# Kernel tuning notes

Measured on AMD Instinct MI355X. Metric: run time of the kernel, lower is better.

The kernel has to match this reference:

```python
import jax, jax.numpy as jnp
import numpy as np

N, E, D, H, L, QD = 100000, 640000, 128, 256, 3, 768


def setup_inputs() -> dict:
    key = jax.random.key(0)
    ks = jax.random.split(key, 16)
    def W(k, shape, fan):
        return jax.random.normal(k, shape, jnp.float32) / np.float32(np.sqrt(fan))
    return {
        "node_embedding": jax.random.normal(ks[0], (N, D), jnp.float32),
        "relation_embedding": jax.random.normal(ks[1], (E, D), jnp.float32),
        "question_embedding": jax.random.normal(ks[2], (1, QD), jnp.float32),
        "edge_index": jax.random.randint(ks[3], (2, E), 0, N),
        "edge_type": jax.random.randint(ks[4], (E,), 0, 2000),
        "qW": W(ks[5], (QD, D), QD),
        "qb": jnp.zeros((D,), jnp.float32),
        "eW1": W(ks[6], (L, 4 * D, H), 4 * D),
        "eb1": jnp.zeros((L, H), jnp.float32),
        "eW2": W(ks[7], (L, H, D), H),
        "eb2": jnp.zeros((L, D), jnp.float32),
        "nW1": W(ks[8], (L, 2 * D, H), 2 * D),
        "nb1": jnp.zeros((L, H), jnp.float32),
        "nW2": W(ks[9], (L, H, D), H),
        "nb2": jnp.zeros((L, D), jnp.float32),
        "esW": W(ks[10], (D, 1), D),
        "esb": jnp.zeros((1,), jnp.float32),
        "nsW": W(ks[11], (D, 1), D),
        "nsb": jnp.zeros((1,), jnp.float32),
    }


def reference(node_embedding, relation_embedding, question_embedding, edge_index,
              edge_type, qW, qb, eW1, eb1, eW2, eb2, nW1, nb1, nW2, nb2,
              esW, esb, nsW, nsb):
    # edge_type is unused in the original forward as well.
    q = question_embedding @ qW + qb  # [1, D]
    src, dst = edge_index[0], edge_index[1]
    node_h = node_embedding  # [N, D]
    edge_h = relation_embedding  # [E, D]
    num_layers = eW1.shape[0]
    for l in range(num_layers):
        edge_src = node_h[src]  # gather [E, D]
        edge_dst = node_h[dst]  # gather [E, D]
        q_exp = jnp.broadcast_to(q, (edge_src.shape[0], q.shape[1]))
        edge_feat = jnp.concatenate([edge_src, edge_dst, edge_h, q_exp], axis=-1)  # [E, 4D]
        h = jax.nn.relu(edge_feat @ eW1[l] + eb1[l])
        edge_h = h @ eW2[l] + eb2[l]  # [E, D]
        # scatter-add to both endpoints (index_add_ on src then dst)
        agg = jnp.zeros_like(node_h).at[src].add(edge_h).at[dst].add(edge_h)
        nh = jax.nn.relu(jnp.concatenate([node_h, agg], axis=-1) @ nW1[l] + nb1[l])
        node_h = nh @ nW2[l] + nb2[l]
    edge_scores = jax.nn.sigmoid((edge_h @ esW + esb).squeeze(-1))  # [E]
    node_scores = jax.nn.sigmoid((node_h @ nsW + nsb).squeeze(-1))  # [N]
    return node_scores, edge_scores
```

## Files before the change

### kernel.cpp

```cpp
#include <hip/hip_runtime.h>
#include <math.h>

#define NN 100000
#define NE 640000
#define DD 128
#define HH 256
#define NL 3
#define QDIM 768
#define TM 64

#define A1P 392
#define A2P 264
#define OP  136

typedef _Float16 h16x8 __attribute__((ext_vector_type(8)));
typedef float f32x4 __attribute__((ext_vector_type(4)));

#define MFMA16(A, B, C) __builtin_amdgcn_mfma_f32_16x16x32_f16(A, B, C, 0, 0, 0)

__device__ __forceinline__ unsigned short f2h_bits(float f) {
    _Float16 h = (_Float16)f;
    return __builtin_bit_cast(unsigned short, h);
}
__device__ __forceinline__ unsigned pk2(float a, float b) {
    return (unsigned)f2h_bits(a) | ((unsigned)f2h_bits(b) << 16);
}
__device__ __forceinline__ float h2f(unsigned short u) {
    return (float)__builtin_bit_cast(_Float16, u);
}

__global__ void q_kernel(const float* __restrict__ qe, const float* __restrict__ qW,
                         const float* __restrict__ qb, float* __restrict__ q) {
    int d = threadIdx.x;
    float acc = qb[d];
    for (int k = 0; k < QDIM; ++k) acc = fmaf(qe[k], qW[k * DD + d], acc);
    q[d] = acc;
}

__global__ void qc_kernel(const float* __restrict__ q, const float* __restrict__ eW1,
                          const float* __restrict__ eb1, float* __restrict__ qc) {
    int l = blockIdx.x;
    int h = threadIdx.x;
    const float* W = eW1 + ((size_t)l * 4 * DD + 3 * DD) * HH;
    __shared__ float sq[DD];
    if (h < DD) sq[h] = q[h];
    __syncthreads();
    float acc = eb1[l * HH + h];
    for (int d = 0; d < DD; ++d) acc = fmaf(sq[d], W[d * HH + h], acc);
    qc[l * HH + h] = acc;
}

__global__ void pack_kernel(const float* __restrict__ W, unsigned short* __restrict__ out,
                            int K, int Ncols, int lstride, size_t plane ) {
    int nct = Ncols >> 4;
    int bx = blockIdx.x;
    int l = blockIdx.y;
    int lane = threadIdx.x;
    const float* Wl = W + (size_t)l * lstride;
    int kt = bx / nct, ct = bx - kt * nct;
    int r = kt * 32 + (lane >> 4) * 8;
    int c = ct * 16 + (lane & 15);
    unsigned vh[4], vl[4];
#pragma unroll
    for (int p = 0; p < 4; ++p) {
        float x0 = Wl[(size_t)(r + 2 * p) * Ncols + c];
        float x1 = Wl[(size_t)(r + 2 * p + 1) * Ncols + c];
        _Float16 h0 = (_Float16)x0, h1 = (_Float16)x1;
        _Float16 l0 = (_Float16)(x0 - (float)h0), l1 = (_Float16)(x1 - (float)h1);
        vh[p] = (unsigned)__builtin_bit_cast(unsigned short, h0) |
                ((unsigned)__builtin_bit_cast(unsigned short, h1) << 16);
        vl[p] = (unsigned)__builtin_bit_cast(unsigned short, l0) |
                ((unsigned)__builtin_bit_cast(unsigned short, l1) << 16);
    }
    size_t off = (size_t)l * K * Ncols + ((size_t)bx * 64 + lane) * 8;
    *(uint4*)(out + off) = make_uint4(vh[0], vh[1], vh[2], vh[3]);
    *(uint4*)(out + plane + off) = make_uint4(vl[0], vl[1], vl[2], vl[3]);
}

__global__ void deg_kernel(const int* __restrict__ eidx, int* __restrict__ cnt) {
    int i = blockIdx.x * 256 + threadIdx.x;
    if (i < 2 * NE) atomicAdd(&cnt[eidx[i]], 1);
}

#define SCAN_T 1024
__global__ void scan_kernel(const int* __restrict__ cnt, int* __restrict__ offsets,
                            int* __restrict__ cursor) {
    __shared__ int s[SCAN_T];
    int t = threadIdx.x;
    const int chunk = (NN + SCAN_T - 1) / SCAN_T;
    int lo = t * chunk, hi = lo + chunk; if (hi > NN) hi = NN;
    int sum = 0;
    for (int i = lo; i < hi; ++i) sum += cnt[i];
    s[t] = sum;
    __syncthreads();
    for (int off = 1; off < SCAN_T; off <<= 1) {
        int v = (t >= off) ? s[t - off] : 0;
        __syncthreads();
        s[t] += v;
        __syncthreads();
    }
    int run = (t == 0) ? 0 : s[t - 1];
    for (int i = lo; i < hi; ++i) {
        int c = cnt[i];
        offsets[i] = run;
        cursor[i] = run;
        run += c;
    }
    if (t == SCAN_T - 1) offsets[NN] = run;
}

__global__ void fill_kernel(const int* __restrict__ eidx, int* __restrict__ cursor,
                            int* __restrict__ inc) {
    int i = blockIdx.x * 256 + threadIdx.x;
    if (i < 2 * NE) {
        int e = (i < NE) ? i : i - NE;
        int pos = atomicAdd(&cursor[eidx[i]], 1);
        inc[pos] = e;
    }
}

template <bool IN16>
__global__ __launch_bounds__(256, 3) void edge_kernel(
    const void* node_in, const void* edge_in,
    unsigned short* edge_out,
    const int* __restrict__ eidx,
    const unsigned short* __restrict__ W1hi, const unsigned short* __restrict__ W1lo,
    const float* __restrict__ qc,
    const unsigned short* __restrict__ W2hi, const unsigned short* __restrict__ W2lo,
    const float* __restrict__ b2)
{
    __shared__ unsigned short sA[TM * A1P];
    unsigned short* sA1 = sA;
    unsigned short* sA2 = sA;
    unsigned short* sOut = sA;

    const int tid = threadIdx.x;
    const int e0 = blockIdx.x * TM;

    const int row = tid >> 2, t4 = tid & 3;
    const int srcn = eidx[e0 + row];
    const int dstn = eidx[NE + e0 + row];

    if (IN16) {
        const unsigned short* b0 = (const unsigned short*)node_in + (size_t)srcn * 256;
        const unsigned short* b1 = (const unsigned short*)node_in + (size_t)dstn * 256;
        const unsigned short* bp = (const unsigned short*)edge_in + (size_t)(e0 + row) * 256;
#pragma unroll
        for (int i = 0; i < 12; ++i) {
            int seg = i >> 2, j = i & 3;
            int c = (t4 + 4 * j) * 8;
            const unsigned short* g = (seg == 0) ? b0 : (seg == 1) ? b1 : bp;
            *(uint4*)&sA1[row * A1P + seg * 128 + c] = *(const uint4*)(g + c);
        }
    } else {
        const float* b0 = (const float*)node_in + (size_t)srcn * DD;
        const float* b1 = (const float*)node_in + (size_t)dstn * DD;
        const float* bp = (const float*)edge_in + (size_t)(e0 + row) * DD;
#pragma unroll
        for (int i = 0; i < 12; ++i) {
            int seg = i >> 2, j = i & 3;
            int c = (t4 + 4 * j) * 8;
            const float* g = (seg == 0) ? b0 : (seg == 1) ? b1 : bp;
            float4 v0 = *(const float4*)(g + c);
            float4 v1 = *(const float4*)(g + c + 4);
            uint4 p = make_uint4(pk2(v0.x, v0.y), pk2(v0.z, v0.w),
                                 pk2(v1.x, v1.y), pk2(v1.z, v1.w));
            *(uint4*)&sA1[row * A1P + seg * 128 + c] = p;
        }
    }

    const int lane = tid & 63;
    const int w = tid >> 6;
    const int lrow = lane & 15;
    const int q4 = lane >> 4;

    f32x4 acc[4][4];
#pragma unroll
    for (int ct = 0; ct < 4; ++ct) {
        float iv = qc[w * 64 + ct * 16 + lrow];
        f32x4 c = {iv, iv, iv, iv};
#pragma unroll
        for (int rt = 0; rt < 4; ++rt) acc[rt][ct] = c;
    }
    __syncthreads();

    const h16x8* W1h = (const h16x8*)W1hi;
    const h16x8* W1l = (const h16x8*)W1lo;
    for (int kt = 0; kt < 12; ++kt) {
        h16x8 a[4];
#pragma unroll
        for (int rt = 0; rt < 4; ++rt)
            a[rt] = *(const h16x8*)&sA1[(lrow + 16 * rt) * A1P + kt * 32 + q4 * 8];
#pragma unroll
        for (int ct = 0; ct < 4; ++ct) {
            h16x8 bh = W1h[(kt * 16 + w * 4 + ct) * 64 + lane];
            h16x8 bl = W1l[(kt * 16 + w * 4 + ct) * 64 + lane];
#pragma unroll
            for (int rt = 0; rt < 4; ++rt) {
                acc[rt][ct] = MFMA16(a[rt], bh, acc[rt][ct]);
                acc[rt][ct] = MFMA16(a[rt], bl, acc[rt][ct]);
            }
        }
    }

    __syncthreads();

#pragma unroll
    for (int rt = 0; rt < 4; ++rt)
#pragma unroll
        for (int ct = 0; ct < 4; ++ct)
#pragma unroll
            for (int j = 0; j < 4; ++j) {
                int hr = rt * 16 + q4 * 4 + j;
                int hc = w * 64 + ct * 16 + lrow;
                sA2[hr * A2P + hc] = f2h_bits(fmaxf(acc[rt][ct][j], 0.0f));
            }
    __syncthreads();

    f32x4 acc2[4][2];
#pragma unroll
    for (int ct = 0; ct < 2; ++ct) {
        float iv = b2[w * 32 + ct * 16 + lrow];
        f32x4 c = {iv, iv, iv, iv};
#pragma unroll
        for (int rt = 0; rt < 4; ++rt) acc2[rt][ct] = c;
    }
    const h16x8* W2h = (const h16x8*)W2hi;
    const h16x8* W2l = (const h16x8*)W2lo;
    for (int kt = 0; kt < 8; ++kt) {
        h16x8 a[4];
#pragma unroll
        for (int rt = 0; rt < 4; ++rt)
            a[rt] = *(const h16x8*)&sA2[(lrow + 16 * rt) * A2P + kt * 32 + q4 * 8];
#pragma unroll
        for (int ct = 0; ct < 2; ++ct) {
            h16x8 bh = W2h[(kt * 8 + w * 2 + ct) * 64 + lane];
            h16x8 bl = W2l[(kt * 8 + w * 2 + ct) * 64 + lane];
#pragma unroll
            for (int rt = 0; rt < 4; ++rt) {
                acc2[rt][ct] = MFMA16(a[rt], bh, acc2[rt][ct]);
                acc2[rt][ct] = MFMA16(a[rt], bl, acc2[rt][ct]);
            }
        }
    }

    __syncthreads();
#pragma unroll
    for (int rt = 0; rt < 4; ++rt)
#pragma unroll
        for (int j = 0; j < 4; ++j) {
            int rr = rt * 16 + q4 * 4 + j;
#pragma unroll
            for (int ct = 0; ct < 2; ++ct)
                sOut[rr * OP + w * 32 + ct * 16 + lrow] = f2h_bits(acc2[rt][ct][j]);
        }
    __syncthreads();
    {
        unsigned short* er = edge_out + (size_t)(e0 + row) * 256;
#pragma unroll
        for (int j = 0; j < 4; ++j)
            *(uint4*)(er + t4 * 32 + j * 8) = *(const uint4*)&sOut[row * OP + t4 * 32 + j * 8];
    }
}

template <bool IN16>
__global__ __launch_bounds__(256, 3) void node_kernel(
    const void* node_in, unsigned short* node_out,
    const unsigned short* __restrict__ edge16,
    const int* __restrict__ offsets, const int* __restrict__ inc,
    const unsigned short* __restrict__ W1hi, const unsigned short* __restrict__ W1lo,
    const float* __restrict__ b1,
    const unsigned short* __restrict__ W2hi, const unsigned short* __restrict__ W2lo,
    const float* __restrict__ b2)
{
    __shared__ unsigned short sA[TM * A2P];
    unsigned short* sA1 = sA;
    unsigned short* sA2 = sA;
    unsigned short* sOut = sA;

    const int tid = threadIdx.x;
    const int n0 = blockIdx.x * TM;

    const int row = tid >> 2, t4 = tid & 3;
    const int n = n0 + row;
    const bool vrow = (n < NN);

    if (vrow) {
        if (IN16) {
            const unsigned short* g0 = (const unsigned short*)node_in + (size_t)n * 256;
#pragma unroll
            for (int j = 0; j < 4; ++j) {
                int c = t4 * 32 + j * 8;
                *(uint4*)&sA1[row * A2P + c] = *(const uint4*)(g0 + c);
            }
        } else {
            const float* g0 = (const float*)node_in + (size_t)n * DD;
#pragma unroll
            for (int j = 0; j < 4; ++j) {
                int c = t4 * 32 + j * 8;
                float4 v0 = *(const float4*)(g0 + c);
                float4 v1 = *(const float4*)(g0 + c + 4);
                uint4 p = make_uint4(pk2(v0.x, v0.y), pk2(v0.z, v0.w),
                                     pk2(v1.x, v1.y), pk2(v1.z, v1.w));
                *(uint4*)&sA1[row * A2P + c] = p;
            }
        }
    } else {
        uint4 z = make_uint4(0, 0, 0, 0);
#pragma unroll
        for (int j = 0; j < 4; ++j)
            *(uint4*)&sA1[row * A2P + t4 * 32 + j * 8] = z;
    }

    {
        int k0 = 0, k1 = 0;
        if (vrow) { k0 = offsets[n]; k1 = offsets[n + 1]; }
        float a[32];
#pragma unroll
        for (int j = 0; j < 32; ++j) a[j] = 0.0f;
        for (int k = k0; k < k1; ++k) {
            int e = inc[k];
            const unsigned short* er = edge16 + (size_t)e * 256 + t4 * 32;
#pragma unroll
            for (int j = 0; j < 4; ++j) {
                uint4 v = *(const uint4*)(er + j * 8);
                a[j * 8 + 0] += h2f((unsigned short)(v.x & 0xffff));
                a[j * 8 + 1] += h2f((unsigned short)(v.x >> 16));
                a[j * 8 + 2] += h2f((unsigned short)(v.y & 0xffff));
                a[j * 8 + 3] += h2f((unsigned short)(v.y >> 16));
                a[j * 8 + 4] += h2f((unsigned short)(v.z & 0xffff));
                a[j * 8 + 5] += h2f((unsigned short)(v.z >> 16));
                a[j * 8 + 6] += h2f((unsigned short)(v.w & 0xffff));
                a[j * 8 + 7] += h2f((unsigned short)(v.w >> 16));
            }
        }
#pragma unroll
        for (int j = 0; j < 4; ++j) {
            uint4 p = make_uint4(pk2(a[j * 8 + 0], a[j * 8 + 1]), pk2(a[j * 8 + 2], a[j * 8 + 3]),
                                 pk2(a[j * 8 + 4], a[j * 8 + 5]), pk2(a[j * 8 + 6], a[j * 8 + 7]));
            *(uint4*)&sA1[row * A2P + 128 + t4 * 32 + j * 8] = p;
        }
    }

    const int lane = tid & 63;
    const int w = tid >> 6;
    const int lrow = lane & 15;
    const int q4 = lane >> 4;

    f32x4 acc[4][4];
#pragma unroll
    for (int ct = 0; ct < 4; ++ct) {
        float iv = b1[w * 64 + ct * 16 + lrow];
        f32x4 c = {iv, iv, iv, iv};
#pragma unroll
        for (int rt = 0; rt < 4; ++rt) acc[rt][ct] = c;
    }
    __syncthreads();

    const h16x8* W1h = (const h16x8*)W1hi;
    const h16x8* W1l = (const h16x8*)W1lo;
    for (int kt = 0; kt < 8; ++kt) {
        h16x8 a[4];
#pragma unroll
        for (int rt = 0; rt < 4; ++rt)
            a[rt] = *(const h16x8*)&sA1[(lrow + 16 * rt) * A2P + kt * 32 + q4 * 8];
#pragma unroll
        for (int ct = 0; ct < 4; ++ct) {
            h16x8 bh = W1h[(kt * 16 + w * 4 + ct) * 64 + lane];
            h16x8 bl = W1l[(kt * 16 + w * 4 + ct) * 64 + lane];
#pragma unroll
            for (int rt = 0; rt < 4; ++rt) {
                acc[rt][ct] = MFMA16(a[rt], bh, acc[rt][ct]);
                acc[rt][ct] = MFMA16(a[rt], bl, acc[rt][ct]);
            }
        }
    }

    __syncthreads();

#pragma unroll
    for (int rt = 0; rt < 4; ++rt)
#pragma unroll
        for (int ct = 0; ct < 4; ++ct)
#pragma unroll
            for (int j = 0; j < 4; ++j) {
                int hr = rt * 16 + q4 * 4 + j;
                int hc = w * 64 + ct * 16 + lrow;
                sA2[hr * A2P + hc] = f2h_bits(fmaxf(acc[rt][ct][j], 0.0f));
            }
    __syncthreads();

    f32x4 acc2[4][2];
#pragma unroll
    for (int ct = 0; ct < 2; ++ct) {
        float iv = b2[w * 32 + ct * 16 + lrow];
        f32x4 c = {iv, iv, iv, iv};
#pragma unroll
        for (int rt = 0; rt < 4; ++rt) acc2[rt][ct] = c;
    }
    const h16x8* W2h = (const h16x8*)W2hi;
    const h16x8* W2l = (const h16x8*)W2lo;
    for (int kt = 0; kt < 8; ++kt) {
        h16x8 a[4];
#pragma unroll
        for (int rt = 0; rt < 4; ++rt)
            a[rt] = *(const h16x8*)&sA2[(lrow + 16 * rt) * A2P + kt * 32 + q4 * 8];
#pragma unroll
        for (int ct = 0; ct < 2; ++ct) {
            h16x8 bh = W2h[(kt * 8 + w * 2 + ct) * 64 + lane];
            h16x8 bl = W2l[(kt * 8 + w * 2 + ct) * 64 + lane];
#pragma unroll
            for (int rt = 0; rt < 4; ++rt) {
                acc2[rt][ct] = MFMA16(a[rt], bh, acc2[rt][ct]);
                acc2[rt][ct] = MFMA16(a[rt], bl, acc2[rt][ct]);
            }
        }
    }

    __syncthreads();
#pragma unroll
    for (int rt = 0; rt < 4; ++rt)
#pragma unroll
        for (int j = 0; j < 4; ++j) {
            int rr = rt * 16 + q4 * 4 + j;
#pragma unroll
            for (int ct = 0; ct < 2; ++ct)
                sOut[rr * OP + w * 32 + ct * 16 + lrow] = f2h_bits(acc2[rt][ct][j]);
        }
    __syncthreads();
    if (vrow) {
        unsigned short* nr = node_out + (size_t)n * 256;
#pragma unroll
        for (int j = 0; j < 4; ++j)
            *(uint4*)(nr + t4 * 32 + j * 8) = *(const uint4*)&sOut[row * OP + t4 * 32 + j * 8];
    }
}

__global__ void score_kernel(const unsigned short* __restrict__ hmat,
                             const float* __restrict__ w,
                             const float* __restrict__ b, float* __restrict__ out) {
    int wid = threadIdx.x >> 6;
    int lane = threadIdx.x & 63;
    int row = blockIdx.x * 4 + wid;
    unsigned v = *(const unsigned*)(hmat + (size_t)row * 256 + lane * 2);
    float2 wv = *(const float2*)(w + lane * 2);
    float s = h2f((unsigned short)(v & 0xffff)) * wv.x +
              h2f((unsigned short)(v >> 16)) * wv.y;
#pragma unroll
    for (int off = 32; off; off >>= 1) s += __shfl_down(s, off);
    if (lane == 0) out[row] = 1.0f / (1.0f + expf(-(s + b[0])));
}

extern "C" void kernel_launch(void* const* d_in, const int* in_sizes, int n_in,
                              void* d_out, int out_size, void* d_ws, size_t ws_size,
                              hipStream_t stream) {
    float* node_h = (float*)d_in[0];
    float* edge_h = (float*)d_in[1];
    const float* qe   = (const float*)d_in[2];
    const int*   eidx = (const int*)d_in[3];
    const float* qW  = (const float*)d_in[5];
    const float* qb  = (const float*)d_in[6];
    const float* eW1 = (const float*)d_in[7];
    const float* eb1 = (const float*)d_in[8];
    const float* eW2 = (const float*)d_in[9];
    const float* eb2 = (const float*)d_in[10];
    const float* nW1 = (const float*)d_in[11];
    const float* nb1 = (const float*)d_in[12];
    const float* nW2 = (const float*)d_in[13];
    const float* nb2 = (const float*)d_in[14];
    const float* esW = (const float*)d_in[15];
    const float* esb = (const float*)d_in[16];
    const float* nsW = (const float*)d_in[17];
    const float* nsb = (const float*)d_in[18];

    unsigned short* nh16 = (unsigned short*)node_h;
    unsigned short* eh16 = (unsigned short*)edge_h;

    float* ws  = (float*)d_ws;
    float* q   = ws;
    float* qc  = ws + 256;
    int* cnt     = (int*)(ws + 1024);
    int* cursor  = cnt + NN;
    int* offsets = cursor + NN;
    int* inc     = offsets + NN + 1;

    unsigned short* packs = (unsigned short*)d_out;
    const size_t pe1 = (size_t)NL * 384 * 256;
    const size_t pe2 = (size_t)NL * 256 * 128;
    const size_t pn1 = (size_t)NL * 256 * 256;
    const size_t pn2 = (size_t)NL * 256 * 128;
    unsigned short* eW1p = packs;
    unsigned short* eW2p = eW1p + 2 * pe1;
    unsigned short* nW1p = eW2p + 2 * pe2;
    unsigned short* nW2p = nW1p + 2 * pn1;

    q_kernel<<<1, DD, 0, stream>>>(qe, qW, qb, q);
    qc_kernel<<<NL, HH, 0, stream>>>(q, eW1, eb1, qc);
    pack_kernel<<<dim3(12 * 16, NL), 64, 0, stream>>>(eW1, eW1p, 384, 256, 4 * DD * HH, pe1);
    pack_kernel<<<dim3(8 * 8, NL), 64, 0, stream>>>(eW2, eW2p, 256, 128, HH * DD, pe2);
    pack_kernel<<<dim3(8 * 16, NL), 64, 0, stream>>>(nW1, nW1p, 256, 256, 2 * DD * HH, pn1);
    pack_kernel<<<dim3(8 * 8, NL), 64, 0, stream>>>(nW2, nW2p, 256, 128, HH * DD, pn2);

    hipMemsetAsync(cnt, 0, NN * sizeof(int), stream);
    deg_kernel<<<(2 * NE + 255) / 256, 256, 0, stream>>>(eidx, cnt);
    scan_kernel<<<1, SCAN_T, 0, stream>>>(cnt, offsets, cursor);
    fill_kernel<<<(2 * NE + 255) / 256, 256, 0, stream>>>(eidx, cursor, inc);

    for (int l = 0; l < NL; ++l) {
        if (l == 0) {
            edge_kernel<false><<<NE / TM, 256, 0, stream>>>(
                (const void*)node_h, (const void*)edge_h, eh16, eidx,
                eW1p + (size_t)l * 384 * 256, eW1p + pe1 + (size_t)l * 384 * 256,
                qc + l * HH,
                eW2p + (size_t)l * 256 * 128, eW2p + pe2 + (size_t)l * 256 * 128,
                eb2 + l * DD);
            node_kernel<false><<<(NN + TM - 1) / TM, 256, 0, stream>>>(
                (const void*)node_h, nh16, eh16, offsets, inc,
                nW1p + (size_t)l * 256 * 256, nW1p + pn1 + (size_t)l * 256 * 256,
                nb1 + l * HH,
                nW2p + (size_t)l * 256 * 128, nW2p + pn2 + (size_t)l * 256 * 128,
                nb2 + l * DD);
        } else {
            edge_kernel<true><<<NE / TM, 256, 0, stream>>>(
                (const void*)nh16, (const void*)eh16, eh16, eidx,
                eW1p + (size_t)l * 384 * 256, eW1p + pe1 + (size_t)l * 384 * 256,
                qc + l * HH,
                eW2p + (size_t)l * 256 * 128, eW2p + pe2 + (size_t)l * 256 * 128,
                eb2 + l * DD);
            node_kernel<true><<<(NN + TM - 1) / TM, 256, 0, stream>>>(
                (const void*)nh16, nh16, eh16, offsets, inc,
                nW1p + (size_t)l * 256 * 256, nW1p + pn1 + (size_t)l * 256 * 256,
                nb1 + l * HH,
                nW2p + (size_t)l * 256 * 128, nW2p + pn2 + (size_t)l * 256 * 128,
                nb2 + l * DD);
        }
    }

    score_kernel<<<NN / 4, 256, 0, stream>>>(nh16, nsW, nsb, (float*)d_out);
    score_kernel<<<NE / 4, 256, 0, stream>>>(eh16, esW, esb, (float*)d_out + NN);
}
```

Baseline: 2.302 ms.

## Stream contiguous operand rows directly from global memory into MFMA, shrink LDS

```diff
diff --git a/kernel.cpp b/kernel.cpp
--- a/kernel.cpp
+++ b/kernel.cpp
@@ -9,8 +9,7 @@
 #define QDIM 768
 #define TM 64
 
-#define A1P 392
-#define A2P 264
+#define EAP 264
 #define OP  136
 
 typedef _Float16 h16x8 __attribute__((ext_vector_type(8)));
@@ -27,6 +26,12 @@
 }
 __device__ __forceinline__ float h2f(unsigned short u) {
     return (float)__builtin_bit_cast(_Float16, u);
+}
+__device__ __forceinline__ h16x8 f4x2_to_h8(float4 v0, float4 v1) {
+    union { unsigned u[4]; h16x8 h; } u;
+    u.u[0] = pk2(v0.x, v0.y); u.u[1] = pk2(v0.z, v0.w);
+    u.u[2] = pk2(v1.x, v1.y); u.u[3] = pk2(v1.z, v1.w);
+    return u.h;
 }
 
 __global__ void q_kernel(const float* __restrict__ qe, const float* __restrict__ qW,
@@ -120,7 +125,7 @@
 }
 
 template <bool IN16>
-__global__ __launch_bounds__(256, 3) void edge_kernel(
+__global__ __launch_bounds__(256, 4) void edge_kernel(
     const void* node_in, const void* edge_in,
     unsigned short* edge_out,
     const int* __restrict__ eidx,
@@ -129,7 +134,7 @@
     const unsigned short* __restrict__ W2hi, const unsigned short* __restrict__ W2lo,
     const float* __restrict__ b2)
 {
-    __shared__ unsigned short sA[TM * A1P];
+    __shared__ unsigned short sA[TM * EAP];
     unsigned short* sA1 = sA;
     unsigned short* sA2 = sA;
     unsigned short* sOut = sA;
@@ -144,28 +149,27 @@
     if (IN16) {
         const unsigned short* b0 = (const unsigned short*)node_in + (size_t)srcn * 256;
         const unsigned short* b1 = (const unsigned short*)node_in + (size_t)dstn * 256;
-        const unsigned short* bp = (const unsigned short*)edge_in + (size_t)(e0 + row) * 256;
-#pragma unroll
-        for (int i = 0; i < 12; ++i) {
-            int seg = i >> 2, j = i & 3;
-            int c = (t4 + 4 * j) * 8;
-            const unsigned short* g = (seg == 0) ? b0 : (seg == 1) ? b1 : bp;
-            *(uint4*)&sA1[row * A1P + seg * 128 + c] = *(const uint4*)(g + c);
+#pragma unroll
+        for (int j = 0; j < 4; ++j) {
+            int c = t4 * 32 + j * 8;
+            *(uint4*)&sA1[row * EAP + c]       = *(const uint4*)(b0 + c);
+            *(uint4*)&sA1[row * EAP + 128 + c] = *(const uint4*)(b1 + c);
         }
     } else {
         const float* b0 = (const float*)node_in + (size_t)srcn * DD;
         const float* b1 = (const float*)node_in + (size_t)dstn * DD;
-        const float* bp = (const float*)edge_in + (size_t)(e0 + row) * DD;
-#pragma unroll
-        for (int i = 0; i < 12; ++i) {
-            int seg = i >> 2, j = i & 3;
-            int c = (t4 + 4 * j) * 8;
-            const float* g = (seg == 0) ? b0 : (seg == 1) ? b1 : bp;
-            float4 v0 = *(const float4*)(g + c);
-            float4 v1 = *(const float4*)(g + c + 4);
-            uint4 p = make_uint4(pk2(v0.x, v0.y), pk2(v0.z, v0.w),
-                                 pk2(v1.x, v1.y), pk2(v1.z, v1.w));
-            *(uint4*)&sA1[row * A1P + seg * 128 + c] = p;
+#pragma unroll
+        for (int s = 0; s < 2; ++s) {
+            const float* g = s ? b1 : b0;
+#pragma unroll
+            for (int j = 0; j < 4; ++j) {
+                int c = t4 * 32 + j * 8;
+                float4 v0 = *(const float4*)(g + c);
+                float4 v1 = *(const float4*)(g + c + 4);
+                uint4 p = make_uint4(pk2(v0.x, v0.y), pk2(v0.z, v0.w),
+                                     pk2(v1.x, v1.y), pk2(v1.z, v1.w));
+                *(uint4*)&sA1[row * EAP + s * 128 + c] = p;
+            }
         }
     }
 
@@ -182,15 +186,44 @@
 #pragma unroll
         for (int rt = 0; rt < 4; ++rt) acc[rt][ct] = c;
     }
-    __syncthreads();
 
     const h16x8* W1h = (const h16x8*)W1hi;
     const h16x8* W1l = (const h16x8*)W1lo;
-    for (int kt = 0; kt < 12; ++kt) {
+
+    for (int kt = 0; kt < 4; ++kt) {
         h16x8 a[4];
+        if (IN16) {
+#pragma unroll
+            for (int rt = 0; rt < 4; ++rt)
+                a[rt] = *(const h16x8*)((const unsigned short*)edge_in +
+                        (size_t)(e0 + lrow + 16 * rt) * 256 + kt * 32 + q4 * 8);
+        } else {
+#pragma unroll
+            for (int rt = 0; rt < 4; ++rt) {
+                const float* g = (const float*)edge_in +
+                        (size_t)(e0 + lrow + 16 * rt) * DD + kt * 32 + q4 * 8;
+                a[rt] = f4x2_to_h8(*(const float4*)g, *(const float4*)(g + 4));
+            }
+        }
+#pragma unroll
+        for (int ct = 0; ct < 4; ++ct) {
+            h16x8 bh = W1h[((kt + 8) * 16 + w * 4 + ct) * 64 + lane];
+            h16x8 bl = W1l[((kt + 8) * 16 + w * 4 + ct) * 64 + lane];
+#pragma unroll
+            for (int rt = 0; rt < 4; ++rt) {
+                acc[rt][ct] = MFMA16(a[rt], bh, acc[rt][ct]);
+                acc[rt][ct] = MFMA16(a[rt], bl, acc[rt][ct]);
+            }
+        }
+    }
+
+    __syncthreads();
+
+    for (int kt = 0; kt < 8; ++kt) {
+        h16x8 a[4];
 #pragma unroll
         for (int rt = 0; rt < 4; ++rt)
-            a[rt] = *(const h16x8*)&sA1[(lrow + 16 * rt) * A1P + kt * 32 + q4 * 8];
+            a[rt] = *(const h16x8*)&sA1[(lrow + 16 * rt) * EAP + kt * 32 + q4 * 8];
 #pragma unroll
         for (int ct = 0; ct < 4; ++ct) {
             h16x8 bh = W1h[(kt * 16 + w * 4 + ct) * 64 + lane];
@@ -213,7 +246,7 @@
             for (int j = 0; j < 4; ++j) {
                 int hr = rt * 16 + q4 * 4 + j;
                 int hc = w * 64 + ct * 16 + lrow;
-                sA2[hr * A2P + hc] = f2h_bits(fmaxf(acc[rt][ct][j], 0.0f));
+                sA2[hr * EAP + hc] = f2h_bits(fmaxf(acc[rt][ct][j], 0.0f));
             }
     __syncthreads();
 
@@ -231,7 +264,7 @@
         h16x8 a[4];
 #pragma unroll
         for (int rt = 0; rt < 4; ++rt)
-            a[rt] = *(const h16x8*)&sA2[(lrow + 16 * rt) * A2P + kt * 32 + q4 * 8];
+            a[rt] = *(const h16x8*)&sA2[(lrow + 16 * rt) * EAP + kt * 32 + q4 * 8];
 #pragma unroll
         for (int ct = 0; ct < 2; ++ct) {
             h16x8 bh = W2h[(kt * 8 + w * 2 + ct) * 64 + lane];
@@ -264,7 +297,7 @@
 }
 
 template <bool IN16>
-__global__ __launch_bounds__(256, 3) void node_kernel(
+__global__ __launch_bounds__(256, 4) void node_kernel(
     const void* node_in, unsigned short* node_out,
     const unsigned short* __restrict__ edge16,
     const int* __restrict__ offsets, const int* __restrict__ inc,
@@ -273,7 +306,7 @@
     const unsigned short* __restrict__ W2hi, const unsigned short* __restrict__ W2lo,
     const float* __restrict__ b2)
 {
-    __shared__ unsigned short sA[TM * A2P];
+    __shared__ unsigned short sA[TM * EAP];
     unsigned short* sA1 = sA;
     unsigned short* sA2 = sA;
     unsigned short* sOut = sA;
@@ -284,33 +317,6 @@
     const int row = tid >> 2, t4 = tid & 3;
     const int n = n0 + row;
     const bool vrow = (n < NN);
-
-    if (vrow) {
-        if (IN16) {
-            const unsigned short* g0 = (const unsigned short*)node_in + (size_t)n * 256;
-#pragma unroll
-            for (int j = 0; j < 4; ++j) {
-                int c = t4 * 32 + j * 8;
-                *(uint4*)&sA1[row * A2P + c] = *(const uint4*)(g0 + c);
-            }
-        } else {
-            const float* g0 = (const float*)node_in + (size_t)n * DD;
-#pragma unroll
-            for (int j = 0; j < 4; ++j) {
-                int c = t4 * 32 + j * 8;
-                float4 v0 = *(const float4*)(g0 + c);
-                float4 v1 = *(const float4*)(g0 + c + 4);
-                uint4 p = make_uint4(pk2(v0.x, v0.y), pk2(v0.z, v0.w),
-                                     pk2(v1.x, v1.y), pk2(v1.z, v1.w));
-                *(uint4*)&sA1[row * A2P + c] = p;
-            }
-        }
-    } else {
-        uint4 z = make_uint4(0, 0, 0, 0);
-#pragma unroll
-        for (int j = 0; j < 4; ++j)
-            *(uint4*)&sA1[row * A2P + t4 * 32 + j * 8] = z;
-    }
 
     {
         int k0 = 0, k1 = 0;
@@ -338,7 +344,7 @@
         for (int j = 0; j < 4; ++j) {
             uint4 p = make_uint4(pk2(a[j * 8 + 0], a[j * 8 + 1]), pk2(a[j * 8 + 2], a[j * 8 + 3]),
                                  pk2(a[j * 8 + 4], a[j * 8 + 5]), pk2(a[j * 8 + 6], a[j * 8 + 7]));
-            *(uint4*)&sA1[row * A2P + 128 + t4 * 32 + j * 8] = p;
+            *(uint4*)&sA1[row * EAP + t4 * 32 + j * 8] = p;
         }
     }
 
@@ -355,15 +361,24 @@
 #pragma unroll
         for (int rt = 0; rt < 4; ++rt) acc[rt][ct] = c;
     }
-    __syncthreads();
 
     const h16x8* W1h = (const h16x8*)W1hi;
     const h16x8* W1l = (const h16x8*)W1lo;
-    for (int kt = 0; kt < 8; ++kt) {
+
+    for (int kt = 0; kt < 4; ++kt) {
         h16x8 a[4];
 #pragma unroll
-        for (int rt = 0; rt < 4; ++rt)
-            a[rt] = *(const h16x8*)&sA1[(lrow + 16 * rt) * A2P + kt * 32 + q4 * 8];
+        for (int rt = 0; rt < 4; ++rt) {
+            int r = n0 + lrow + 16 * rt;
+            if (r > NN - 1) r = NN - 1;
+            if (IN16) {
+                a[rt] = *(const h16x8*)((const unsigned short*)node_in +
+                        (size_t)r * 256 + kt * 32 + q4 * 8);
+            } else {
+                const float* g = (const float*)node_in + (size_t)r * DD + kt * 32 + q4 * 8;
+                a[rt] = f4x2_to_h8(*(const float4*)g, *(const float4*)(g + 4));
+            }
+        }
 #pragma unroll
         for (int ct = 0; ct < 4; ++ct) {
             h16x8 bh = W1h[(kt * 16 + w * 4 + ct) * 64 + lane];
@@ -378,6 +393,25 @@
 
     __syncthreads();
 
+    for (int kt = 0; kt < 4; ++kt) {
+        h16x8 a[4];
+#pragma unroll
+        for (int rt = 0; rt < 4; ++rt)
+            a[rt] = *(const h16x8*)&sA1[(lrow + 16 * rt) * EAP + kt * 32 + q4 * 8];
+#pragma unroll
+        for (int ct = 0; ct < 4; ++ct) {
+            h16x8 bh = W1h[((kt + 4) * 16 + w * 4 + ct) * 64 + lane];
+            h16x8 bl = W1l[((kt + 4) * 16 + w * 4 + ct) * 64 + lane];
+#pragma unroll
+            for (int rt = 0; rt < 4; ++rt) {
+                acc[rt][ct] = MFMA16(a[rt], bh, acc[rt][ct]);
+                acc[rt][ct] = MFMA16(a[rt], bl, acc[rt][ct]);
+            }
+        }
+    }
+
+    __syncthreads();
+
 #pragma unroll
     for (int rt = 0; rt < 4; ++rt)
 #pragma unroll
@@ -386,7 +420,7 @@
             for (int j = 0; j < 4; ++j) {
                 int hr = rt * 16 + q4 * 4 + j;
                 int hc = w * 64 + ct * 16 + lrow;
-                sA2[hr * A2P + hc] = f2h_bits(fmaxf(acc[rt][ct][j], 0.0f));
+                sA2[hr * EAP + hc] = f2h_bits(fmaxf(acc[rt][ct][j], 0.0f));
             }
     __syncthreads();
 
@@ -404,7 +438,7 @@
         h16x8 a[4];
 #pragma unroll
         for (int rt = 0; rt < 4; ++rt)
-            a[rt] = *(const h16x8*)&sA2[(lrow + 16 * rt) * A2P + kt * 32 + q4 * 8];
+            a[rt] = *(const h16x8*)&sA2[(lrow + 16 * rt) * EAP + kt * 32 + q4 * 8];
 #pragma unroll
         for (int ct = 0; ct < 2; ++ct) {
             h16x8 bh = W2h[(kt * 8 + w * 2 + ct) * 64 + lane];
```

Result: slower. 2.457 ms (+6.7%).
